# Performance work log

Hardware: AMD Instinct MI355X
Metric: run time of the kernel (lower is better)

Reference implementation:

```python
import jax, jax.numpy as jnp
import numpy as np

T, B, IN, H, A = 512, 256, 292, 128, 12


def setup_inputs() -> dict:
    key = jax.random.key(0)
    ks = jax.random.split(key, 8)
    s = 1.0 / np.sqrt(H)
    return {
        "x": jax.random.normal(ks[0], (T, B, IN), dtype=jnp.float32),
        "done": jax.random.randint(ks[1], (T, B), 0, 2, dtype=jnp.int32),
        "h0": jax.random.normal(ks[2], (1, B, H), dtype=jnp.float32),
        "c0": jax.random.normal(ks[3], (1, B, H), dtype=jnp.float32),
        "W_ih": jax.random.normal(ks[4], (4 * H, IN), dtype=jnp.float32) * s,
        "W_hh": jax.random.normal(ks[5], (4 * H, H), dtype=jnp.float32) * s,
        "b_ih": jnp.zeros((4 * H,), dtype=jnp.float32),
        "b_hh": jnp.zeros((4 * H,), dtype=jnp.float32),
        "W_pi": jax.random.normal(ks[6], (A, H), dtype=jnp.float32) * 0.01,
        "b_pi": jnp.zeros((A,), dtype=jnp.float32),
        "W_v": jax.random.normal(ks[7], (1, H), dtype=jnp.float32),
        "b_v": jnp.zeros((1,), dtype=jnp.float32),
    }


def reference(x, done, h0, c0, W_ih, W_hh, b_ih, b_hh, W_pi, b_pi, W_v, b_v):
    # get_states: per-timestep LSTM with done-based reset of (h, c), as a scan.
    done_f = done.astype(x.dtype)  # [T, B]
    bias = b_ih + b_hh  # [4H]

    def step(carry, inp):
        h, c = carry  # [B, H] each
        x_t, d_t = inp  # [B, IN], [B]
        m = (1.0 - d_t)[:, None]  # reset mask
        h = h * m
        c = c * m
        # PyTorch LSTM gate order: input, forget, cell(g), output
        gates = x_t @ W_ih.T + h @ W_hh.T + bias  # [B, 4H]
        i, f, g, o = jnp.split(gates, 4, axis=-1)
        c = jax.nn.sigmoid(f) * c + jax.nn.sigmoid(i) * jnp.tanh(g)
        h = jax.nn.sigmoid(o) * jnp.tanh(c)
        return (h, c), h

    (hN, cN), hs = jax.lax.scan(step, (h0[0], c0[0]), (x, done_f))
    hidden = hs.reshape(T * B, H)  # flatten(cat(new_hidden), 0, 1)
    logits = hidden @ W_pi.T + b_pi  # policy_layers
    value = hidden @ W_v.T + b_v  # value_layers
    return jnp.concatenate([logits, value], axis=-1)  # [T*B, A+1]
```

## Files before the change

### kernel.cpp

```cpp
#include <hip/hip_runtime.h>
#include <stdint.h>
#include <stddef.h>

#define T_ 512
#define B_ 256
#define IN_ 292
#define H_ 128
#define G4_ 512
#define TB_ 131072
#define LCH 32
#define NCH 16
#define KP_ 320

typedef short bf16x8 __attribute__((ext_vector_type(8)));
typedef float f32x4 __attribute__((ext_vector_type(4)));

__device__ __forceinline__ unsigned short f2bf(float f) {
  unsigned u = __float_as_uint(f);
  u += 0x7FFFu + ((u >> 16) & 1u);
  return (unsigned short)(u >> 16);
}
__device__ __forceinline__ float bf2f(unsigned short s) {
  return __uint_as_float(((unsigned)s) << 16);
}
__device__ __forceinline__ unsigned bfpack2(float a, float b) {
  unsigned ua = __float_as_uint(a) + 0x8000u;
  unsigned ub = __float_as_uint(b) + 0x8000u;
  return __builtin_amdgcn_perm(ub, ua, 0x07060302u);
}
__device__ __forceinline__ float sigf(float x) {
  return __builtin_amdgcn_rcpf(1.0f + __expf(-x));
}
__device__ __forceinline__ float tanhf_(float x) {
  return 1.0f - 2.0f * __builtin_amdgcn_rcpf(__expf(2.0f * x) + 1.0f);
}
__device__ __forceinline__ void barrier_lds() {
  asm volatile("s_waitcnt lgkmcnt(0)\n\ts_barrier" ::: "memory");
}
__device__ __forceinline__ void gload_lds16(const float* g, float* l) {
  __builtin_amdgcn_global_load_lds(
      (const __attribute__((address_space(1))) void*)g,
      (__attribute__((address_space(3))) void*)l, 16, 0, 0);
}
__device__ __forceinline__ void load_pr(const unsigned short* p, ushort4* pr) {
  union { uint4 v; ushort4 s[2]; } a, b;
  a.v = *(const uint4*)p;
  b.v = *(const uint4*)(p + 8);
  pr[0] = a.s[0]; pr[1] = a.s[1]; pr[2] = b.s[0]; pr[3] = b.s[1];
}

__global__ __launch_bounds__(256) void k0w_cvt(
    const float* __restrict__ Wih, const float* __restrict__ bih,
    const float* __restrict__ bhh, unsigned short* __restrict__ Wf,
    float* __restrict__ bias2) {
  const int g = blockIdx.x * 256 + threadIdx.x;
  const int lane = g & 63;
  const int rest = g >> 6;
  const int it = rest % 10;
  const int g16 = rest / 10;
  const int jj = g16 * 16 + (lane & 15);
  const int src = (jj & 3) * 128 + (jj >> 2);
  const int c0 = it * 32 + (lane >> 4) * 8;
  if (g < 512) {
    const int sb = (g & 3) * 128 + (g >> 2);
    bias2[g] = bih[sb] + bhh[sb];
  }
  float4 a = {0.f, 0.f, 0.f, 0.f}, b = {0.f, 0.f, 0.f, 0.f};
  const float* p = Wih + (size_t)src * IN_ + c0;
  if (c0 + 8 <= IN_) { a = *(const float4*)p; b = *(const float4*)(p + 4); }
  else if (c0 < IN_) { a = *(const float4*)p; }
  uint4 o;
  o.x = bfpack2(a.x, a.y); o.y = bfpack2(a.z, a.w);
  o.z = bfpack2(b.x, b.y); o.w = bfpack2(b.z, b.w);
  *(uint4*)&Wf[(size_t)g * 8] = o;
}

__device__ __forceinline__ void k1_stage(
    const float* __restrict__ x, float* ldsbuf, int bid4, int g2,
    int w, int lane) {
  const int jx = g2 / 10, kt = g2 % 10;
#pragma unroll
  for (int j = 0; j < 2; ++j) {
    const int r = w * 16 + j * 8 + (lane >> 3);
    const int tq = (lane & 7) ^ (r & 7);
    const float* src =
        x + (size_t)((bid4 + jx) * 128 + r) * IN_ + kt * 32 + tq * 4;
    float* dst = ldsbuf + w * 512 + j * 256;
    if (kt < 9 || tq == 0) gload_lds16(src, dst);
  }
}

__global__ __launch_bounds__(512, 2) void k1_pregemm(
    const float* __restrict__ x, const unsigned short* __restrict__ Wf,
    const float* __restrict__ bias2, unsigned short* __restrict__ pre2) {
  __shared__ float xtf[2][128 * 32];
  __shared__ unsigned short ep[64 * 520];

  const int tid = threadIdx.x;
  const int w = tid >> 6;
  const int lane = tid & 63;
  const int l15 = lane & 15;
  const int q = lane >> 4;
  const int bid4 = blockIdx.x * 4;

  const unsigned short* wfbase = Wf + ((size_t)(4 * w) * 10 * 64 + lane) * 8;

  f32x4 acc[4][8];
#pragma unroll
  for (int s = 0; s < 4; s++)
#pragma unroll
    for (int ms = 0; ms < 8; ms++) acc[s][ms] = (f32x4){0.f, 0.f, 0.f, 0.f};

  k1_stage(x, &xtf[0][0], bid4, 0, w, lane);
  bf16x8 af[4];
#pragma unroll
  for (int s = 0; s < 4; s++)
    af[s] = *(const bf16x8*)(wfbase + (s * 10 + 0) * 512);
  __syncthreads();

#pragma unroll 1
  for (int git = 0; git < 40; ++git) {
    const int kt = git % 10;
    bf16x8 afn[4];
    if (git < 39) {
      const int nit = (kt == 9) ? 0 : kt + 1;
#pragma unroll
      for (int s = 0; s < 4; s++)
        afn[s] = *(const bf16x8*)(wfbase + (s * 10 + nit) * 512);
    }
    const float* xb = &xtf[git & 1][0];
    bf16x8 bfr[8];
#pragma unroll
    for (int ms = 0; ms < 8; ms++) {
      const int r = 16 * ms + l15;
      const int a0 = (2 * q) ^ (r & 7), a1 = (2 * q + 1) ^ (r & 7);
      const float4 u0 = *(const float4*)&xb[r * 32 + a0 * 4];
      const float4 u1 = *(const float4*)&xb[r * 32 + a1 * 4];
      union { unsigned u[4]; bf16x8 v; } cv;
      cv.u[0] = bfpack2(u0.x, u0.y); cv.u[1] = bfpack2(u0.z, u0.w);
      cv.u[2] = bfpack2(u1.x, u1.y); cv.u[3] = bfpack2(u1.z, u1.w);
      bfr[ms] = cv.v;
    }
    if (git < 39) k1_stage(x, &xtf[(git + 1) & 1][0], bid4, git + 1, w, lane);
#pragma unroll
    for (int s = 0; s < 4; s++)
#pragma unroll
      for (int ms = 0; ms < 8; ms++)
        acc[s][ms] = __builtin_amdgcn_mfma_f32_16x16x32_bf16(
            af[s], bfr[ms], acc[s][ms], 0, 0, 0);
#pragma unroll
    for (int s = 0; s < 4; s++) af[s] = afn[s];
    __syncthreads();

    if (kt == 9) {
      const int m0 = (bid4 + git / 10) * 128;
      float4 bb[4];
#pragma unroll
      for (int s = 0; s < 4; s++)
        bb[s] = *(const float4*)&bias2[64 * w + 16 * s + 4 * q];
#pragma unroll
      for (int st = 0; st < 2; ++st) {
#pragma unroll
        for (int mm = 0; mm < 4; ++mm) {
          const int ms = 4 * st + mm;
#pragma unroll
          for (int s = 0; s < 4; ++s) {
            uint2 v;
            v.x = bfpack2(acc[s][ms][0] + bb[s].x, acc[s][ms][1] + bb[s].y);
            v.y = bfpack2(acc[s][ms][2] + bb[s].z, acc[s][ms][3] + bb[s].w);
            *(uint2*)&ep[(16 * mm + l15) * 520 + 64 * w + 16 * s + 4 * q] = v;
          }
        }
        barrier_lds();
#pragma unroll
        for (int p = 0; p < 8; ++p) {
          const int r = 8 * p + w;
          uint4 v = *(const uint4*)&ep[r * 520 + lane * 8];
          *(uint4*)&pre2[((size_t)(m0 + 64 * st + r) << 9) + lane * 8] = v;
        }
        barrier_lds();
      }
      if (git < 39) {
#pragma unroll
        for (int s = 0; s < 4; s++)
#pragma unroll
          for (int ms = 0; ms < 8; ms++) acc[s][ms] = (f32x4){0.f, 0.f, 0.f, 0.f};
      }
    }
  }
}

__global__ __launch_bounds__(512) void k2a_chunk(
    const unsigned short* __restrict__ pre2, const float* __restrict__ Whh,
    const int* __restrict__ done, unsigned short* __restrict__ hidden,
    unsigned short* __restrict__ hfin, float* __restrict__ cfin) {
  __shared__ unsigned short hs[2][16 * 136];
  __shared__ int dns[LCH * 16];

  const int bg = blockIdx.x & 15;
  const int ck = blockIdx.x >> 4;
  const int t0 = ck * LCH;
  const int tid = threadIdx.x;
  const int w = tid >> 6;
  const int lane = tid & 63;
  const int l15 = lane & 15;
  const int q = lane >> 4;
  const int bglob = bg * 16 + l15;
  const int kcell = 16 * w + 4 * q;
  const int kq16 = kcell * 4;

  {
    const int r = tid >> 4, c = tid & 15;
    dns[tid] = done[(size_t)(t0 + r) * B_ + bg * 16 + c];
  }

  bf16x8 wf[4][4];
#pragma unroll
  for (int tI = 0; tI < 4; tI++) {
    const int jg = 16 * (w + 8 * tI) + l15;
#pragma unroll
    for (int kc = 0; kc < 4; kc++) {
      const float* p = Whh + (size_t)jg * H_ + kc * 32 + q * 8;
      float4 u0 = *(const float4*)p;
      float4 u1 = *(const float4*)(p + 4);
      bf16x8 r;
      r[0]=(short)f2bf(u0.x); r[1]=(short)f2bf(u0.y); r[2]=(short)f2bf(u0.z); r[3]=(short)f2bf(u0.w);
      r[4]=(short)f2bf(u1.x); r[5]=(short)f2bf(u1.y); r[6]=(short)f2bf(u1.z); r[7]=(short)f2bf(u1.w);
      wf[tI][kc] = r;
    }
  }

  float c_[4] = {0.f, 0.f, 0.f, 0.f};
  {
    const int b = tid >> 5, k = (tid & 31) * 4;
    *(ushort4*)&hs[0][b * 136 + k] = (ushort4){0, 0, 0, 0};
  }
  bool vld = false;
  __syncthreads();

  ushort4 pr[4], prn[4];
  load_pr(pre2 + ((size_t)t0 * B_ + bglob) * G4_ + kq16, pr);
  load_pr(pre2 + ((size_t)(t0 + 1) * B_ + bglob) * G4_ + kq16, prn);

  ushort4 hw = {0, 0, 0, 0};
#pragma unroll 1
  for (int u = 0; u < LCH; u++) {
    const int t = t0 + u;
    ushort4 pr2[4];
    const int un = (u + 2 < LCH) ? u + 2 : LCH - 1;
    load_pr(pre2 + ((size_t)(t0 + un) * B_ + bglob) * G4_ + kq16, pr2);

    const int dn = dns[u * 16 + l15];
    vld = vld || (dn != 0);

    const unsigned short* hb = hs[u & 1];
    bf16x8 hf[4];
#pragma unroll
    for (int kc = 0; kc < 4; kc++) {
      bf16x8 v = *(const bf16x8*)&hb[l15 * 136 + kc * 32 + q * 8];
      if (dn) v = (bf16x8){0, 0, 0, 0, 0, 0, 0, 0};
      hf[kc] = v;
    }

    f32x4 acc[4];
#pragma unroll
    for (int tI = 0; tI < 4; tI++) acc[tI] = (f32x4){0.f, 0.f, 0.f, 0.f};
#pragma unroll
    for (int tI = 0; tI < 4; tI++)
#pragma unroll
      for (int kc = 0; kc < 4; kc++)
        acc[tI] = __builtin_amdgcn_mfma_f32_16x16x32_bf16(
            wf[tI][kc], hf[kc], acc[tI], 0, 0, 0);

    const float m = dn ? 0.0f : 1.0f;
    float hv[4];
#pragma unroll
    for (int r = 0; r < 4; r++) {
      const float iv = acc[0][r] + bf2f(pr[r].x);
      const float fv = acc[1][r] + bf2f(pr[r].y);
      const float gv = acc[2][r] + bf2f(pr[r].z);
      const float ov = acc[3][r] + bf2f(pr[r].w);
      float cc = c_[r] * m;
      cc = sigf(fv) * cc + sigf(iv) * tanhf_(gv);
      c_[r] = cc;
      hv[r] = sigf(ov) * tanhf_(cc);
    }
    uint2 hp = {bfpack2(hv[0], hv[1]), bfpack2(hv[2], hv[3])};
    hw = *(ushort4*)&hp;
    *(uint2*)&hs[(u + 1) & 1][l15 * 136 + kcell] = hp;
    if (vld)
      *(uint2*)&hidden[((size_t)t * B_ + bglob) * H_ + kcell] = hp;
#pragma unroll
    for (int tI = 0; tI < 4; tI++) { pr[tI] = prn[tI]; prn[tI] = pr2[tI]; }
    barrier_lds();
  }

  *(ushort4*)&hfin[((size_t)ck * B_ + bglob) * H_ + kcell] = hw;
  float4 cv = {c_[0], c_[1], c_[2], c_[3]};
  *(float4*)&cfin[((size_t)ck * B_ + bglob) * H_ + kcell] = cv;
}

__global__ __launch_bounds__(512) void k2b_par(
    const unsigned short* __restrict__ pre2, const float* __restrict__ Whh,
    const float* __restrict__ h0, const float* __restrict__ c0,
    const int* __restrict__ done, unsigned short* __restrict__ hidden,
    const unsigned short* __restrict__ hfin, const float* __restrict__ cfin,
    int* __restrict__ needfix) {
  __shared__ unsigned short hs[2][16 * 136];
  __shared__ int dns[LCH * 16];

  const int bg = blockIdx.x & 15;
  const int ck = blockIdx.x >> 4;
  const int t0 = ck * LCH;
  const int tid = threadIdx.x;
  const int w = tid >> 6;
  const int lane = tid & 63;
  const int l15 = lane & 15;
  const int q = lane >> 4;
  const int bglob = bg * 16 + l15;
  const int kcell = 16 * w + 4 * q;
  const int kq16 = kcell * 4;

  {
    const int r = tid >> 4, c = tid & 15;
    dns[tid] = done[(size_t)(t0 + r) * B_ + bg * 16 + c];
  }

  bf16x8 wf[4][4];
#pragma unroll
  for (int tI = 0; tI < 4; tI++) {
    const int jg = 16 * (w + 8 * tI) + l15;
#pragma unroll
    for (int kc = 0; kc < 4; kc++) {
      const float* p = Whh + (size_t)jg * H_ + kc * 32 + q * 8;
      float4 u0 = *(const float4*)p;
      float4 u1 = *(const float4*)(p + 4);
      bf16x8 r;
      r[0]=(short)f2bf(u0.x); r[1]=(short)f2bf(u0.y); r[2]=(short)f2bf(u0.z); r[3]=(short)f2bf(u0.w);
      r[4]=(short)f2bf(u1.x); r[5]=(short)f2bf(u1.y); r[6]=(short)f2bf(u1.z); r[7]=(short)f2bf(u1.w);
      wf[tI][kc] = r;
    }
  }

  float c_[4];
  {
    const int b = tid >> 5, k = (tid & 31) * 4;
    if (ck == 0) {
      float4 hv = *(const float4*)(h0 + (size_t)(bg * 16 + b) * H_ + k);
      uint2 hp = {bfpack2(hv.x, hv.y), bfpack2(hv.z, hv.w)};
      *(uint2*)&hs[0][b * 136 + k] = hp;
      float4 cv = *(const float4*)(c0 + (size_t)bglob * H_ + kcell);
      c_[0] = cv.x; c_[1] = cv.y; c_[2] = cv.z; c_[3] = cv.w;
    } else {
      ushort4 hv = *(const ushort4*)&hfin[((size_t)(ck - 1) * B_ + bg * 16 + b) * H_ + k];
      *(ushort4*)&hs[0][b * 136 + k] = hv;
      float4 cv = *(const float4*)&cfin[((size_t)(ck - 1) * B_ + bglob) * H_ + kcell];
      c_[0] = cv.x; c_[1] = cv.y; c_[2] = cv.z; c_[3] = cv.w;
    }
  }
  int cur = 0;
  bool act = true;
  __syncthreads();

  ushort4 pr[4];
  load_pr(pre2 + ((size_t)t0 * B_ + bglob) * G4_ + kq16, pr);

#pragma unroll 1
  for (int u = 0; u < LCH; u++) {
    const int t = t0 + u;
    const int dn = dns[u * 16 + l15];
    const bool nact = act && (dn == 0);
    if (__ballot(nact) == 0ULL) { act = false; break; }
    act = nact;

    ushort4 prn[4];
    const int un = (u + 1 < LCH) ? u + 1 : LCH - 1;
    load_pr(pre2 + ((size_t)(t0 + un) * B_ + bglob) * G4_ + kq16, prn);

    const unsigned short* hb = hs[cur];
    bf16x8 hf[4];
#pragma unroll
    for (int kc = 0; kc < 4; kc++)
      hf[kc] = *(const bf16x8*)&hb[l15 * 136 + kc * 32 + q * 8];

    f32x4 acc[4];
#pragma unroll
    for (int tI = 0; tI < 4; tI++) acc[tI] = (f32x4){0.f, 0.f, 0.f, 0.f};
#pragma unroll
    for (int tI = 0; tI < 4; tI++)
#pragma unroll
      for (int kc = 0; kc < 4; kc++)
        acc[tI] = __builtin_amdgcn_mfma_f32_16x16x32_bf16(
            wf[tI][kc], hf[kc], acc[tI], 0, 0, 0);

    float hv[4];
#pragma unroll
    for (int r = 0; r < 4; r++) {
      const float iv = acc[0][r] + bf2f(pr[r].x);
      const float fv = acc[1][r] + bf2f(pr[r].y);
      const float gv = acc[2][r] + bf2f(pr[r].z);
      const float ov = acc[3][r] + bf2f(pr[r].w);
      float cc = sigf(fv) * c_[r] + sigf(iv) * tanhf_(gv);
      c_[r] = cc;
      hv[r] = sigf(ov) * tanhf_(cc);
    }
    uint2 hp = {bfpack2(hv[0], hv[1]), bfpack2(hv[2], hv[3])};
    *(uint2*)&hs[cur ^ 1][l15 * 136 + kcell] = hp;
    if (act)
      *(uint2*)&hidden[((size_t)t * B_ + bglob) * H_ + kcell] = hp;
#pragma unroll
    for (int tI = 0; tI < 4; tI++) pr[tI] = prn[tI];
    barrier_lds();
    cur ^= 1;
  }

  if (tid == 0) needfix[blockIdx.x] = (__ballot(act) != 0ULL) ? 1 : 0;
}

__global__ __launch_bounds__(512) void k2c_guard(
    const unsigned short* __restrict__ pre2, const float* __restrict__ Whh,
    const float* __restrict__ h0, const float* __restrict__ c0,
    const int* __restrict__ done, unsigned short* __restrict__ hidden,
    const unsigned short* __restrict__ hfin, const float* __restrict__ cfin,
    const int* __restrict__ needfix) {
  const int bg = blockIdx.x;
  bool dirty = false;
  for (int c2 = 0; c2 < NCH - 1; c2++) dirty |= (needfix[c2 * 16 + bg] != 0);
  if (!dirty) return;

  __shared__ unsigned short hs[2][16 * 136];
  __shared__ int dns[T_ * 16];

  const int tid = threadIdx.x;
  const int w = tid >> 6;
  const int lane = tid & 63;
  const int l15 = lane & 15;
  const int q = lane >> 4;
  const int bglob = bg * 16 + l15;
  const int kcell = 16 * w + 4 * q;
  const int kq16 = kcell * 4;

  {
    const int* p = done + (size_t)tid * B_ + bg * 16;
    *(int4*)&dns[tid * 16]      = *(const int4*)(p);
    *(int4*)&dns[tid * 16 + 4]  = *(const int4*)(p + 4);
    *(int4*)&dns[tid * 16 + 8]  = *(const int4*)(p + 8);
    *(int4*)&dns[tid * 16 + 12] = *(const int4*)(p + 12);
  }

  bf16x8 wf[4][4];
#pragma unroll
  for (int tI = 0; tI < 4; tI++) {
    const int jg = 16 * (w + 8 * tI) + l15;
#pragma unroll
    for (int kc = 0; kc < 4; kc++) {
      const float* p = Whh + (size_t)jg * H_ + kc * 32 + q * 8;
      float4 u0 = *(const float4*)p;
      float4 u1 = *(const float4*)(p + 4);
      bf16x8 r;
      r[0]=(short)f2bf(u0.x); r[1]=(short)f2bf(u0.y); r[2]=(short)f2bf(u0.z); r[3]=(short)f2bf(u0.w);
      r[4]=(short)f2bf(u1.x); r[5]=(short)f2bf(u1.y); r[6]=(short)f2bf(u1.z); r[7]=(short)f2bf(u1.w);
      wf[tI][kc] = r;
    }
  }

  float c_[4];
  {
    float4 cv = *(const float4*)(c0 + (size_t)bglob * H_ + kcell);
    c_[0] = cv.x; c_[1] = cv.y; c_[2] = cv.z; c_[3] = cv.w;
    const int b = tid >> 5, k = (tid & 31) * 4;
    float4 hv = *(const float4*)(h0 + (size_t)(bg * 16 + b) * H_ + k);
    uint2 hp = {bfpack2(hv.x, hv.y), bfpack2(hv.z, hv.w)};
    *(uint2*)&hs[0][b * 136 + k] = hp;
  }
  int cur = 0;
  __syncthreads();

#pragma unroll 1
  for (int ck = 0; ck < NCH; ck++) {
    const int t0 = ck * LCH;
    bool act = true;

    ushort4 pr[4];
    load_pr(pre2 + ((size_t)t0 * B_ + bglob) * G4_ + kq16, pr);

#pragma unroll 1
    for (int u = 0; u < LCH; u++) {
      const int t = t0 + u;
      const int dn = dns[t * 16 + l15];
      const bool nact = act && (dn == 0);
      if (__ballot(nact) == 0ULL) { act = false; break; }
      act = nact;

      ushort4 prn[4];
      const int un = (u + 1 < LCH) ? u + 1 : LCH - 1;
      load_pr(pre2 + ((size_t)(t0 + un) * B_ + bglob) * G4_ + kq16, prn);

      const unsigned short* hb = hs[cur];
      bf16x8 hf[4];
#pragma unroll
      for (int kc = 0; kc < 4; kc++)
        hf[kc] = *(const bf16x8*)&hb[l15 * 136 + kc * 32 + q * 8];

      f32x4 acc[4];
#pragma unroll
      for (int tI = 0; tI < 4; tI++) acc[tI] = (f32x4){0.f, 0.f, 0.f, 0.f};
#pragma unroll
      for (int tI = 0; tI < 4; tI++)
#pragma unroll
        for (int kc = 0; kc < 4; kc++)
          acc[tI] = __builtin_amdgcn_mfma_f32_16x16x32_bf16(
              wf[tI][kc], hf[kc], acc[tI], 0, 0, 0);

      float hv[4];
#pragma unroll
      for (int r = 0; r < 4; r++) {
        const float iv = acc[0][r] + bf2f(pr[r].x);
        const float fv = acc[1][r] + bf2f(pr[r].y);
        const float gv = acc[2][r] + bf2f(pr[r].z);
        const float ov = acc[3][r] + bf2f(pr[r].w);
        float cc = sigf(fv) * c_[r] + sigf(iv) * tanhf_(gv);
        c_[r] = cc;
        hv[r] = sigf(ov) * tanhf_(cc);
      }
      uint2 hp = {bfpack2(hv[0], hv[1]), bfpack2(hv[2], hv[3])};
      *(uint2*)&hs[cur ^ 1][l15 * 136 + kcell] = hp;
      if (act)
        *(uint2*)&hidden[((size_t)t * B_ + bglob) * H_ + kcell] = hp;
#pragma unroll
      for (int tI = 0; tI < 4; tI++) pr[tI] = prn[tI];
      barrier_lds();
      cur ^= 1;
    }

    if (!act) {
      ushort4 hv = *(const ushort4*)&hfin[((size_t)ck * B_ + bglob) * H_ + kcell];
      float4 cv = *(const float4*)&cfin[((size_t)ck * B_ + bglob) * H_ + kcell];
      c_[0] = cv.x; c_[1] = cv.y; c_[2] = cv.z; c_[3] = cv.w;
      *(ushort4*)&hs[cur][l15 * 136 + kcell] = hv;
    }
    barrier_lds();
  }
}

__global__ __launch_bounds__(256) void k3_head(
    const unsigned short* __restrict__ hidden, const float* __restrict__ Wpi,
    const float* __restrict__ bpi, const float* __restrict__ Wv,
    const float* __restrict__ bv, float* __restrict__ out) {
  __shared__ unsigned short hs3[64 * 136];
  __shared__ float bias_s[16];

  const int tid = threadIdx.x;
  const int w = tid >> 6;
  const int lane = tid & 63;
  const int l15 = lane & 15;
  const int q = lane >> 4;
  const int m0 = blockIdx.x * 64;

  if (tid < 16) bias_s[tid] = (tid < 12) ? bpi[tid] : ((tid == 12) ? bv[0] : 0.f);

  bf16x8 wf3[4];
#pragma unroll
  for (int kc = 0; kc < 4; kc++) {
    float4 u0 = {0.f, 0.f, 0.f, 0.f}, u1 = {0.f, 0.f, 0.f, 0.f};
    if (l15 < 12) {
      const float* p = Wpi + (size_t)l15 * H_ + kc * 32 + q * 8;
      u0 = *(const float4*)p; u1 = *(const float4*)(p + 4);
    } else if (l15 == 12) {
      const float* p = Wv + kc * 32 + q * 8;
      u0 = *(const float4*)p; u1 = *(const float4*)(p + 4);
    }
    bf16x8 r;
    r[0]=(short)f2bf(u0.x); r[1]=(short)f2bf(u0.y); r[2]=(short)f2bf(u0.z); r[3]=(short)f2bf(u0.w);
    r[4]=(short)f2bf(u1.x); r[5]=(short)f2bf(u1.y); r[6]=(short)f2bf(u1.z); r[7]=(short)f2bf(u1.w);
    wf3[kc] = r;
  }

  {
    const int row = tid >> 2, ks = (tid & 3) * 32;
    const unsigned short* p = hidden + (size_t)(m0 + row) * H_ + ks;
#pragma unroll
    for (int i = 0; i < 4; i++)
      *(uint4*)&hs3[row * 136 + ks + i * 8] = *(const uint4*)(p + i * 8);
  }
  __syncthreads();

  f32x4 acc = (f32x4){0.f, 0.f, 0.f, 0.f};
#pragma unroll
  for (int kc = 0; kc < 4; kc++) {
    bf16x8 hf = *(bf16x8*)&hs3[(16 * w + l15) * 136 + kc * 32 + q * 8];
    acc = __builtin_amdgcn_mfma_f32_16x16x32_bf16(wf3[kc], hf, acc, 0, 0, 0);
  }

  const float4 bb = *(float4*)&bias_s[4 * q];
  const int m = m0 + 16 * w + l15;
  const size_t ro = (size_t)m * 13;
  float v0 = acc[0] + bb.x, v1 = acc[1] + bb.y, v2 = acc[2] + bb.z, v3 = acc[3] + bb.w;
  if (q < 3) {
    out[ro + 4 * q + 0] = v0;
    out[ro + 4 * q + 1] = v1;
    out[ro + 4 * q + 2] = v2;
    out[ro + 4 * q + 3] = v3;
  } else {
    out[ro + 12] = v0;
  }
}

extern "C" void kernel_launch(void* const* d_in, const int* in_sizes, int n_in,
                              void* d_out, int out_size, void* d_ws, size_t ws_size,
                              hipStream_t stream) {
  const float* x    = (const float*)d_in[0];
  const int* done   = (const int*)d_in[1];
  const float* h0   = (const float*)d_in[2];
  const float* c0   = (const float*)d_in[3];
  const float* Wih  = (const float*)d_in[4];
  const float* Whh  = (const float*)d_in[5];
  const float* bih  = (const float*)d_in[6];
  const float* bhh  = (const float*)d_in[7];
  const float* Wpi  = (const float*)d_in[8];
  const float* bpi  = (const float*)d_in[9];
  const float* Wv   = (const float*)d_in[10];
  const float* bv   = (const float*)d_in[11];
  (void)in_sizes; (void)n_in; (void)out_size; (void)ws_size;

  unsigned short* pre2 = (unsigned short*)d_ws;
  unsigned short* hidden = pre2 + (size_t)TB_ * G4_;
  unsigned short* Wf   = (unsigned short*)d_out;
  float* bias2         = (float*)((char*)d_out + (512u << 10));
  unsigned short* hfin = (unsigned short*)((char*)d_out + (1u << 20));
  float* cfin          = (float*)((char*)d_out + (2u << 20));
  int* needfix         = (int*)((char*)d_out + (4u << 20));
  float* out = (float*)d_out;

  k0w_cvt<<<80, 256, 0, stream>>>(Wih, bih, bhh, Wf, bias2);
  k1_pregemm<<<256, 512, 0, stream>>>(x, Wf, bias2, pre2);
  k2a_chunk<<<256, 512, 0, stream>>>(pre2, Whh, done, hidden, hfin, cfin);
  k2b_par<<<256, 512, 0, stream>>>(pre2, Whh, h0, c0, done, hidden, hfin, cfin, needfix);
  k2c_guard<<<16, 512, 0, stream>>>(pre2, Whh, h0, c0, done, hidden, hfin, cfin, needfix);
  k3_head<<<TB_ / 64, 256, 0, stream>>>(hidden, Wpi, bpi, Wv, bv, out);
}
```

Measured before the change: 380.5 us.

## Halve recurrence chunk length and give pre-GEMM one tile per wide block

The input-projection GEMM moves from 256 blocks of 512 threads, each looping over four 128-row tiles, to 1024 blocks of 1024 threads, each handling one 128-row tile with the waves split into two row halves. This is meant to give more parallelism and a smaller epilogue staging buffer. The chunked LSTM recurrence now uses 32 chunks of 16 steps instead of 16 chunks of 32, doubling the blocks available for the parallel-chunk scheme, and k2b prefetches pre-activations two steps ahead. Workspace offsets are repacked to fit. Shorter chunks may make the guard/fix path run more often and raise per-block setup overhead.

```diff
diff --git a/kernel.cpp b/kernel.cpp
--- a/kernel.cpp
+++ b/kernel.cpp
@@ -8,8 +8,8 @@
 #define H_ 128
 #define G4_ 512
 #define TB_ 131072
-#define LCH 32
-#define NCH 16
+#define LCH 16
+#define NCH 32
 #define KP_ 320
 
 typedef short bf16x8 __attribute__((ext_vector_type(8)));
@@ -75,43 +75,34 @@
   *(uint4*)&Wf[(size_t)g * 8] = o;
 }
 
-__device__ __forceinline__ void k1_stage(
-    const float* __restrict__ x, float* ldsbuf, int bid4, int g2,
-    int w, int lane) {
-  const int jx = g2 / 10, kt = g2 % 10;
-#pragma unroll
-  for (int j = 0; j < 2; ++j) {
-    const int r = w * 16 + j * 8 + (lane >> 3);
-    const int tq = (lane & 7) ^ (r & 7);
-    const float* src =
-        x + (size_t)((bid4 + jx) * 128 + r) * IN_ + kt * 32 + tq * 4;
-    float* dst = ldsbuf + w * 512 + j * 256;
-    if (kt < 9 || tq == 0) gload_lds16(src, dst);
-  }
-}
-
-__global__ __launch_bounds__(512, 2) void k1_pregemm(
+__global__ __launch_bounds__(1024, 8) void k1_pregemm(
     const float* __restrict__ x, const unsigned short* __restrict__ Wf,
     const float* __restrict__ bias2, unsigned short* __restrict__ pre2) {
   __shared__ float xtf[2][128 * 32];
-  __shared__ unsigned short ep[64 * 520];
+  __shared__ unsigned short ep[16 * 520];
 
   const int tid = threadIdx.x;
   const int w = tid >> 6;
+  const int wr = w >> 3;
+  const int wc = w & 7;
   const int lane = tid & 63;
   const int l15 = lane & 15;
   const int q = lane >> 4;
-  const int bid4 = blockIdx.x * 4;
-
-  const unsigned short* wfbase = Wf + ((size_t)(4 * w) * 10 * 64 + lane) * 8;
-
-  f32x4 acc[4][8];
+  const int m0 = blockIdx.x * 128;
+
+  const unsigned short* wfbase = Wf + ((size_t)(4 * wc) * 10 * 64 + lane) * 8;
+
+  const int srow = tid >> 3;
+  const int stq = (lane & 7) ^ (lane >> 3);
+  const float* xrowp = x + (size_t)(m0 + srow) * IN_ + stq * 4;
+
+  f32x4 acc[4][4];
 #pragma unroll
   for (int s = 0; s < 4; s++)
 #pragma unroll
-    for (int ms = 0; ms < 8; ms++) acc[s][ms] = (f32x4){0.f, 0.f, 0.f, 0.f};
-
-  k1_stage(x, &xtf[0][0], bid4, 0, w, lane);
+    for (int ms = 0; ms < 4; ms++) acc[s][ms] = (f32x4){0.f, 0.f, 0.f, 0.f};
+
+  gload_lds16(xrowp, &xtf[0][0] + w * 256);
   bf16x8 af[4];
 #pragma unroll
   for (int s = 0; s < 4; s++)
@@ -119,20 +110,22 @@
   __syncthreads();
 
 #pragma unroll 1
-  for (int git = 0; git < 40; ++git) {
-    const int kt = git % 10;
+  for (int kt = 0; kt < 10; ++kt) {
     bf16x8 afn[4];
-    if (git < 39) {
-      const int nit = (kt == 9) ? 0 : kt + 1;
+    if (kt < 9) {
 #pragma unroll
       for (int s = 0; s < 4; s++)
-        afn[s] = *(const bf16x8*)(wfbase + (s * 10 + nit) * 512);
-    }
-    const float* xb = &xtf[git & 1][0];
-    bf16x8 bfr[8];
-#pragma unroll
-    for (int ms = 0; ms < 8; ms++) {
-      const int r = 16 * ms + l15;
+        afn[s] = *(const bf16x8*)(wfbase + (s * 10 + kt + 1) * 512);
+    }
+    if (kt + 1 < 10) {
+      if (kt + 1 < 9 || stq == 0)
+        gload_lds16(xrowp + (kt + 1) * 32, &xtf[(kt + 1) & 1][0] + w * 256);
+    }
+    const float* xb = &xtf[kt & 1][0];
+    bf16x8 bfr[4];
+#pragma unroll
+    for (int ms = 0; ms < 4; ms++) {
+      const int r = 64 * wr + 16 * ms + l15;
       const int a0 = (2 * q) ^ (r & 7), a1 = (2 * q + 1) ^ (r & 7);
       const float4 u0 = *(const float4*)&xb[r * 32 + a0 * 4];
       const float4 u1 = *(const float4*)&xb[r * 32 + a1 * 4];
@@ -141,52 +134,41 @@
       cv.u[2] = bfpack2(u1.x, u1.y); cv.u[3] = bfpack2(u1.z, u1.w);
       bfr[ms] = cv.v;
     }
-    if (git < 39) k1_stage(x, &xtf[(git + 1) & 1][0], bid4, git + 1, w, lane);
 #pragma unroll
     for (int s = 0; s < 4; s++)
 #pragma unroll
-      for (int ms = 0; ms < 8; ms++)
+      for (int ms = 0; ms < 4; ms++)
         acc[s][ms] = __builtin_amdgcn_mfma_f32_16x16x32_bf16(
             af[s], bfr[ms], acc[s][ms], 0, 0, 0);
 #pragma unroll
     for (int s = 0; s < 4; s++) af[s] = afn[s];
     __syncthreads();
-
-    if (kt == 9) {
-      const int m0 = (bid4 + git / 10) * 128;
-      float4 bb[4];
-#pragma unroll
-      for (int s = 0; s < 4; s++)
-        bb[s] = *(const float4*)&bias2[64 * w + 16 * s + 4 * q];
-#pragma unroll
-      for (int st = 0; st < 2; ++st) {
-#pragma unroll
-        for (int mm = 0; mm < 4; ++mm) {
-          const int ms = 4 * st + mm;
-#pragma unroll
-          for (int s = 0; s < 4; ++s) {
-            uint2 v;
-            v.x = bfpack2(acc[s][ms][0] + bb[s].x, acc[s][ms][1] + bb[s].y);
-            v.y = bfpack2(acc[s][ms][2] + bb[s].z, acc[s][ms][3] + bb[s].w);
-            *(uint2*)&ep[(16 * mm + l15) * 520 + 64 * w + 16 * s + 4 * q] = v;
-          }
-        }
-        barrier_lds();
-#pragma unroll
-        for (int p = 0; p < 8; ++p) {
-          const int r = 8 * p + w;
-          uint4 v = *(const uint4*)&ep[r * 520 + lane * 8];
-          *(uint4*)&pre2[((size_t)(m0 + 64 * st + r) << 9) + lane * 8] = v;
-        }
-        barrier_lds();
+  }
+
+  float4 bb[4];
+#pragma unroll
+  for (int s = 0; s < 4; s++)
+    bb[s] = *(const float4*)&bias2[64 * wc + 16 * s + 4 * q];
+
+#pragma unroll
+  for (int st = 0; st < 8; ++st) {
+    if ((st >> 2) == wr) {
+      const int ms = st & 3;
+#pragma unroll
+      for (int s = 0; s < 4; ++s) {
+        uint2 v;
+        v.x = bfpack2(acc[s][ms][0] + bb[s].x, acc[s][ms][1] + bb[s].y);
+        v.y = bfpack2(acc[s][ms][2] + bb[s].z, acc[s][ms][3] + bb[s].w);
+        *(uint2*)&ep[l15 * 520 + 64 * wc + 16 * s + 4 * q] = v;
       }
-      if (git < 39) {
-#pragma unroll
-        for (int s = 0; s < 4; s++)
-#pragma unroll
-          for (int ms = 0; ms < 8; ms++) acc[s][ms] = (f32x4){0.f, 0.f, 0.f, 0.f};
-      }
-    }
+    }
+    barrier_lds();
+    {
+      uint4 v = *(const uint4*)&ep[w * 520 + lane * 8];
+      const int row = m0 + 64 * (st >> 2) + 16 * (st & 3) + w;
+      *(uint4*)&pre2[((size_t)row << 9) + lane * 8] = v;
+    }
+    barrier_lds();
   }
 }
 
@@ -209,7 +191,7 @@
   const int kcell = 16 * w + 4 * q;
   const int kq16 = kcell * 4;
 
-  {
+  if (tid < LCH * 16) {
     const int r = tid >> 4, c = tid & 15;
     dns[tid] = done[(size_t)(t0 + r) * B_ + bg * 16 + c];
   }
@@ -321,7 +303,7 @@
   const int kcell = 16 * w + 4 * q;
   const int kq16 = kcell * 4;
 
-  {
+  if (tid < LCH * 16) {
     const int r = tid >> 4, c = tid & 15;
     dns[tid] = done[(size_t)(t0 + r) * B_ + bg * 16 + c];
   }
@@ -362,8 +344,9 @@
   bool act = true;
   __syncthreads();
 
-  ushort4 pr[4];
+  ushort4 pr[4], prn[4];
   load_pr(pre2 + ((size_t)t0 * B_ + bglob) * G4_ + kq16, pr);
+  load_pr(pre2 + ((size_t)(t0 + 1) * B_ + bglob) * G4_ + kq16, prn);
 
 #pragma unroll 1
   for (int u = 0; u < LCH; u++) {
@@ -373,9 +356,9 @@
     if (__ballot(nact) == 0ULL) { act = false; break; }
     act = nact;
 
-    ushort4 prn[4];
-    const int un = (u + 1 < LCH) ? u + 1 : LCH - 1;
-    load_pr(pre2 + ((size_t)(t0 + un) * B_ + bglob) * G4_ + kq16, prn);
+    ushort4 pr2[4];
+    const int un = (u + 2 < LCH) ? u + 2 : LCH - 1;
+    load_pr(pre2 + ((size_t)(t0 + un) * B_ + bglob) * G4_ + kq16, pr2);
 
     const unsigned short* hb = hs[cur];
     bf16x8 hf[4];
@@ -409,7 +392,7 @@
     if (act)
       *(uint2*)&hidden[((size_t)t * B_ + bglob) * H_ + kcell] = hp;
 #pragma unroll
-    for (int tI = 0; tI < 4; tI++) pr[tI] = prn[tI];
+    for (int tI = 0; tI < 4; tI++) { pr[tI] = prn[tI]; prn[tI] = pr2[tI]; }
     barrier_lds();
     cur ^= 1;
   }
@@ -626,16 +609,16 @@
   unsigned short* pre2 = (unsigned short*)d_ws;
   unsigned short* hidden = pre2 + (size_t)TB_ * G4_;
   unsigned short* Wf   = (unsigned short*)d_out;
-  float* bias2         = (float*)((char*)d_out + (512u << 10));
-  unsigned short* hfin = (unsigned short*)((char*)d_out + (1u << 20));
-  float* cfin          = (float*)((char*)d_out + (2u << 20));
-  int* needfix         = (int*)((char*)d_out + (4u << 20));
+  float* bias2         = (float*)((char*)d_out + 327680u);
+  int* needfix         = (int*)((char*)d_out + 331776u);
+  unsigned short* hfin = (unsigned short*)((char*)d_out + 524288u);
+  float* cfin          = (float*)((char*)d_out + 2621440u);
   float* out = (float*)d_out;
 
   k0w_cvt<<<80, 256, 0, stream>>>(Wih, bih, bhh, Wf, bias2);
-  k1_pregemm<<<256, 512, 0, stream>>>(x, Wf, bias2, pre2);
-  k2a_chunk<<<256, 512, 0, stream>>>(pre2, Whh, done, hidden, hfin, cfin);
-  k2b_par<<<256, 512, 0, stream>>>(pre2, Whh, h0, c0, done, hidden, hfin, cfin, needfix);
+  k1_pregemm<<<TB_ / 128, 1024, 0, stream>>>(x, Wf, bias2, pre2);
+  k2a_chunk<<<NCH * 16, 512, 0, stream>>>(pre2, Whh, done, hidden, hfin, cfin);
+  k2b_par<<<NCH * 16, 512, 0, stream>>>(pre2, Whh, h0, c0, done, hidden, hfin, cfin, needfix);
   k2c_guard<<<16, 512, 0, stream>>>(pre2, Whh, h0, c0, done, hidden, hfin, cfin, needfix);
   k3_head<<<TB_ / 64, 256, 0, stream>>>(hidden, Wpi, bpi, Wv, bv, out);
 }
```

After: 1.306 ms. +243.2%, slower.
